# Performance work log

Hardware: AMD Instinct MI355X
Metric: run time of the kernel (lower is better)

## Reference

```python
import jax, jax.numpy as jnp
import numpy as np

N_NODES = 50000
N_EDGES = 800000
IN_CH = 64
HID = 128


def setup_inputs() -> dict:
    key = jax.random.key(0)
    ks = jax.random.split(key, 10)
    x = jax.random.normal(ks[0], (N_NODES, IN_CH), dtype=jnp.float32)
    edge_index = jax.random.randint(ks[1], (2, N_EDGES), 0, N_NODES, dtype=jnp.int64)
    def lin(k, fan_in, fan_out):
        bound = 1.0 / np.sqrt(fan_in)
        kw, kb = jax.random.split(k)
        W = jax.random.uniform(kw, (fan_in, fan_out), minval=-bound, maxval=bound, dtype=jnp.float32)
        b = jax.random.uniform(kb, (fan_out,), minval=-bound, maxval=bound, dtype=jnp.float32)
        return W, b
    W1a, b1a = lin(ks[2], 2 * IN_CH, HID)
    W1b, b1b = lin(ks[3], HID, HID)
    W2a, b2a = lin(ks[4], 2 * HID, HID)
    W2b, b2b = lin(ks[5], HID, HID)
    return {"x": x, "edge_index": edge_index,
            "W1a": W1a, "b1a": b1a, "W1b": W1b, "b1b": b1b,
            "W2a": W2a, "b2a": b2a, "W2b": W2b, "b2b": b2b}


def _edge_conv(x, src, dst, Wa, ba, Wb, bb):
    # PyG EdgeConv: message = MLP([x_i, x_j - x_i]), aggr = max at target i (dst)
    xi = x[dst]                                   # [E, C] target feats
    xj = x[src]                                   # [E, C] source feats
    m = jnp.concatenate([xi, xj - xi], axis=-1)   # [E, 2C]
    m = jax.nn.relu(m @ Wa + ba) @ Wb + bb        # [E, H]
    agg = jax.ops.segment_max(m, dst, num_segments=N_NODES)
    # nodes with no incoming edge -> 0 (torch_scatter fill value)
    return jnp.where(jnp.isfinite(agg), agg, 0.0)


def reference(x, edge_index, W1a, b1a, W1b, b1b, W2a, b2a, W2b, b2b):
    src = edge_index[0]
    dst = edge_index[1]
    h = _edge_conv(x, src, dst, W1a, b1a, W1b, b1b)
    h = jax.nn.relu(h)
    h = _edge_conv(h, src, dst, W2a, b2a, W2b, b2b)
    return h
```

## Files before the change

### kernel.cpp

```cpp
#include <hip/hip_runtime.h>
#include <stdint.h>

#define N_NODES 50000
#define N_EDGES 800000
#define HID 128
#define NWG_E (N_EDGES / 128)
#define XQ (NWG_E / 8)
#define XR (NWG_E % 8)
#define SCAN_B 196

#define ENC_NEG_INF 0x007FFFFFu

typedef short short8 __attribute__((ext_vector_type(8)));
typedef float f32x4 __attribute__((ext_vector_type(4)));

__device__ __forceinline__ unsigned enc_f32(float f) {
    unsigned u = __float_as_uint(f);
    return (u & 0x80000000u) ? ~u : (u | 0x80000000u);
}
__device__ __forceinline__ float dec_f32(unsigned e) {
    unsigned u = (e & 0x80000000u) ? (e & 0x7FFFFFFFu) : ~e;
    return __uint_as_float(u);
}
__device__ __forceinline__ unsigned short f2bf(float f) {
    unsigned u = __float_as_uint(f);
    unsigned r = (u + 0x7fffu + ((u >> 16) & 1u)) >> 16;
    return (unsigned short)r;
}
__device__ __forceinline__ float bf2f(unsigned short h) {
    return __uint_as_float(((unsigned)h) << 16);
}


__global__ void fill_u32(unsigned* __restrict__ p, int n, unsigned v) {
    int i = blockIdx.x * blockDim.x + threadIdx.x;
    int stride = gridDim.x * blockDim.x;
    for (; i < n; i += stride) p[i] = v;
}

__global__ void prep_wcat(const float* __restrict__ W, int K, float* __restrict__ WC) {
    int idx = blockIdx.x * 256 + threadIdx.x;
    if (idx >= K * 256) return;
    int k = idx >> 8, c = idx & 255;
    float v;
    if (c < 128) v = W[k * 128 + c] - W[(k + K) * 128 + c];
    else         v = W[(k + K) * 128 + (c - 128)];
    WC[idx] = v;
}

__global__ void prep_wfrag(const float* __restrict__ Wb, unsigned short* __restrict__ Wg) {
    int idx = blockIdx.x * 256 + threadIdx.x;
    int j = idx & 7, l = (idx >> 3) & 63, t = idx >> 9;
    int h = t >> 4, kt = (t >> 2) & 3, ntl = t & 3;
    int nt = 4 * h + ntl;
    int k = 32 * kt + 8 * (l >> 4) + j;
    int n = 16 * nt + (l & 15);
    Wg[idx] = f2bf(Wb[k * 128 + n]);
}

__global__ void prep_wfrag256(const float* __restrict__ WC, int K, unsigned short* __restrict__ Wg) {
    int idx = blockIdx.x * 256 + threadIdx.x;
    if (idx >= K * 256) return;
    int j = idx & 7, l = (idx >> 3) & 63, nt = (idx >> 9) & 15, kt = idx >> 13;
    int k = 32 * kt + 8 * (l >> 4) + j;
    int n = 16 * nt + (l & 15);
    float v = WC[k * 256 + n];
    unsigned short hi = f2bf(v);
    Wg[idx] = hi;
    Wg[K * 256 + idx] = f2bf(v - bf2f(hi));
}

__global__ void out_decode(unsigned* __restrict__ p, const float* __restrict__ bias, int n) {
    int i = blockIdx.x * blockDim.x + threadIdx.x;
    int stride = gridDim.x * blockDim.x;
    for (; i < n; i += stride) {
        unsigned e = p[i];
        float f = (e == ENC_NEG_INF) ? 0.0f : dec_f32(e) + bias[i & 127];
        ((float*)p)[i] = f;
    }
}


__global__ void hist_dst(const int* __restrict__ dst, unsigned* __restrict__ count) {
    int i = blockIdx.x * blockDim.x + threadIdx.x;
    if (i < N_EDGES) atomicAdd(&count[dst[i]], 1u);
}

__global__ __launch_bounds__(256) void scan_p1(const unsigned* __restrict__ count,
                                               unsigned* __restrict__ bsum) {
    __shared__ unsigned s[256];
    int t = threadIdx.x;
    int i = blockIdx.x * 256 + t;
    s[t] = (i < N_NODES) ? count[i] : 0u;
    __syncthreads();
    for (int off = 128; off > 0; off >>= 1) {
        if (t < off) s[t] += s[t + off];
        __syncthreads();
    }
    if (t == 0) bsum[blockIdx.x] = s[0];
}

__global__ __launch_bounds__(256) void scan_p2(unsigned* __restrict__ bsum) {
    __shared__ unsigned s[256];
    int t = threadIdx.x;
    unsigned v = (t < SCAN_B) ? bsum[t] : 0u;
    s[t] = v;
    __syncthreads();
    for (int off = 1; off < 256; off <<= 1) {
        unsigned x = (t >= off) ? s[t - off] : 0u;
        __syncthreads();
        s[t] += x;
        __syncthreads();
    }
    if (t < SCAN_B) bsum[t] = s[t] - v;
}

__global__ __launch_bounds__(256) void scan_p3(const unsigned* __restrict__ count,
                                               const unsigned* __restrict__ bsum,
                                               unsigned* __restrict__ cursor) {
    __shared__ unsigned s[256];
    int t = threadIdx.x;
    int i = blockIdx.x * 256 + t;
    unsigned v = (i < N_NODES) ? count[i] : 0u;
    s[t] = v;
    __syncthreads();
    for (int off = 1; off < 256; off <<= 1) {
        unsigned x = (t >= off) ? s[t - off] : 0u;
        __syncthreads();
        s[t] += x;
        __syncthreads();
    }
    if (i < N_NODES) cursor[i] = bsum[blockIdx.x] + s[t] - v;
}

__global__ void scatter_edges(const int* __restrict__ src, const int* __restrict__ dst,
                              unsigned* __restrict__ cursor,
                              int* __restrict__ ssrc, int* __restrict__ sdst) {
    int i = blockIdx.x * blockDim.x + threadIdx.x;
    if (i < N_EDGES) {
        int d = dst[i];
        unsigned p = atomicAdd(&cursor[d], 1u);
        ssrc[p] = src[i];
        sdst[p] = d;
    }
}

template<int DEC, int KT>
__global__ __launch_bounds__(256, 2) void gemm_uv_mfma(
        const void* __restrict__ A_,
        const unsigned short* __restrict__ Wg,
        const float* __restrict__ bprev,
        const float* __restrict__ bu,
        unsigned short* __restrict__ C,
        int M) {
    __shared__ char lds[KT * 8192];
    const int K = 32 * KT;
    int tid = threadIdx.x;
    int bx = blockIdx.x, by = blockIdx.y;
    int r0 = bx * 128;
    int w = tid >> 6, l = tid & 63;
    int q = l >> 4, m = l & 15;

    short8 ahi[2][KT];
#pragma unroll
    for (int mt = 0; mt < 2; ++mt) {
        int row = r0 + 32 * w + 16 * mt + m;
        bool ok = row < M;
#pragma unroll
        for (int kt = 0; kt < KT; ++kt) {
            float av[8] = {0.f, 0.f, 0.f, 0.f, 0.f, 0.f, 0.f, 0.f};
            if (ok) {
                if (DEC) {
                    const unsigned* Ar = (const unsigned*)A_ + (size_t)row * K + 32 * kt + 8 * q;
                    uint4 x0 = *(const uint4*)Ar;
                    uint4 x1 = *(const uint4*)(Ar + 4);
                    float4 g0 = *(const float4*)&bprev[32 * kt + 8 * q];
                    float4 g1 = *(const float4*)&bprev[32 * kt + 8 * q + 4];
                    av[0] = fmaxf(dec_f32(x0.x) + g0.x, 0.f);
                    av[1] = fmaxf(dec_f32(x0.y) + g0.y, 0.f);
                    av[2] = fmaxf(dec_f32(x0.z) + g0.z, 0.f);
                    av[3] = fmaxf(dec_f32(x0.w) + g0.w, 0.f);
                    av[4] = fmaxf(dec_f32(x1.x) + g1.x, 0.f);
                    av[5] = fmaxf(dec_f32(x1.y) + g1.y, 0.f);
                    av[6] = fmaxf(dec_f32(x1.z) + g1.z, 0.f);
                    av[7] = fmaxf(dec_f32(x1.w) + g1.w, 0.f);
                } else {
                    const float* Ar = (const float*)A_ + (size_t)row * K + 32 * kt + 8 * q;
                    float4 f0 = *(const float4*)Ar;
                    float4 f1 = *(const float4*)(Ar + 4);
                    av[0] = f0.x; av[1] = f0.y; av[2] = f0.z; av[3] = f0.w;
                    av[4] = f1.x; av[5] = f1.y; av[6] = f1.z; av[7] = f1.w;
                }
            }
            short8 hi;
#pragma unroll
            for (int j = 0; j < 8; ++j) hi[j] = (short)f2bf(av[j]);
            ahi[mt][kt] = hi;
        }
    }

    f32x4 acc[2][8];
#pragma unroll
    for (int mt = 0; mt < 2; ++mt)
#pragma unroll
        for (int nt = 0; nt < 8; ++nt)
            acc[mt][nt] = (f32x4){0.f, 0.f, 0.f, 0.f};

    const short8* bfr = (const short8*)lds;

#pragma unroll
    for (int pl = 0; pl < 2; ++pl) {
        if (pl) __syncthreads();
        {
            const float4* s4 = (const float4*)Wg + (size_t)pl * (K * 32);
            float4* d4 = (float4*)lds;
#pragma unroll
            for (int it = 0; it < 2 * KT; ++it) {
                int f = 256 * it + tid;
                int tl = f >> 6, fin = f & 63;
                int tg = (tl >> 3) * 16 + 8 * by + (tl & 7);
                d4[f] = s4[tg * 64 + fin];
            }
        }
        __syncthreads();
#pragma unroll
        for (int nt = 0; nt < 8; ++nt)
#pragma unroll
            for (int kt = 0; kt < KT; ++kt) {
                short8 b = bfr[(kt * 8 + nt) * 64 + l];
                acc[0][nt] = __builtin_amdgcn_mfma_f32_16x16x32_bf16(ahi[0][kt], b, acc[0][nt], 0, 0, 0);
                acc[1][nt] = __builtin_amdgcn_mfma_f32_16x16x32_bf16(ahi[1][kt], b, acc[1][nt], 0, 0, 0);
            }
    }

#pragma unroll
    for (int nt = 0; nt < 8; ++nt) {
        float bias = (by == 0) ? bu[16 * nt + m] : 0.f;
#pragma unroll
        for (int mt = 0; mt < 2; ++mt) {
            int rowb = r0 + 32 * w + 16 * mt + 4 * q;
#pragma unroll
            for (int r = 0; r < 4; ++r) {
                int row = rowb + r;
                if (row < M)
                    C[(size_t)row * 256 + 128 * by + 16 * nt + m] = f2bf(acc[mt][nt][r] + bias);
            }
        }
    }
}

__global__ __launch_bounds__(256, 5) void edge_mlp_mfma(
        const unsigned short* __restrict__ UV,
        const unsigned short* __restrict__ Wg,
        const int* __restrict__ ssrc,
        const int* __restrict__ sdst,
        unsigned* __restrict__ AGG) {
    __shared__ char lds[17408];
    __shared__ int sdst_s[128];
    int tid = threadIdx.x;
    int orig = blockIdx.x;
    int xcd = orig & 7, ii = orig >> 3;
    int wg = (xcd < XR) ? xcd * (XQ + 1) + ii : XR * (XQ + 1) + (xcd - XR) * XQ + ii;
    int e0 = wg * 128;
    int w = tid >> 6, l = tid & 63;
    int q = l >> 4, m = l & 15;

    if (tid < 128) sdst_s[tid] = sdst[e0 + tid];

    short8 ahi[2][4];
    {
        int eA = e0 + 32 * w + m;
        int d0 = sdst[eA], s0 = ssrc[eA];
        int d1 = sdst[eA + 16], s1 = ssrc[eA + 16];
#pragma unroll
        for (int mt = 0; mt < 2; ++mt) {
            int d = mt ? d1 : d0, s = mt ? s1 : s0;
            const short8* Ud = (const short8*)&UV[(size_t)d * 256];
            const short8* Vs = (const short8*)&UV[(size_t)s * 256 + 128];
            short8 u0 = Ud[q],      u1 = Ud[4 + q],  u2 = Ud[8 + q],  u3 = Ud[12 + q];
            short8 v0 = Vs[q],      v1 = Vs[4 + q],  v2 = Vs[8 + q],  v3 = Vs[12 + q];
            short8 ub[4] = {u0, u1, u2, u3};
            short8 vb[4] = {v0, v1, v2, v3};
#pragma unroll
            for (int kt = 0; kt < 4; ++kt) {
                short8 hi;
#pragma unroll
                for (int j = 0; j < 8; ++j) {
                    float t = bf2f((unsigned short)ub[kt][j]) + bf2f((unsigned short)vb[kt][j]);
                    hi[j] = (short)f2bf(fmaxf(t, 0.f));
                }
                ahi[mt][kt] = hi;
            }
        }
    }

    const short8* bfr = (const short8*)lds;
    float* M2 = (float*)lds;
    f32x4 acc[2][4];

#pragma unroll
    for (int h = 0; h < 2; ++h) {
        __syncthreads();
        {
            const float4* s4 = (const float4*)Wg + h * 1024;
            float4* d4 = (float4*)lds;
#pragma unroll
            for (int i = 0; i < 4; ++i) d4[tid + 256 * i] = s4[tid + 256 * i];
        }
        __syncthreads();
#pragma unroll
        for (int mt = 0; mt < 2; ++mt)
#pragma unroll
            for (int ntl = 0; ntl < 4; ++ntl)
                acc[mt][ntl] = (f32x4){0.f, 0.f, 0.f, 0.f};
#pragma unroll
        for (int ntl = 0; ntl < 4; ++ntl)
#pragma unroll
            for (int kt = 0; kt < 4; ++kt) {
                short8 b = bfr[(kt * 4 + ntl) * 64 + l];
                acc[0][ntl] = __builtin_amdgcn_mfma_f32_16x16x32_bf16(ahi[0][kt], b, acc[0][ntl], 0, 0, 0);
                acc[1][ntl] = __builtin_amdgcn_mfma_f32_16x16x32_bf16(ahi[1][kt], b, acc[1][ntl], 0, 0, 0);
            }

#pragma unroll
        for (int cn = 0; cn < 2; ++cn) {
            __syncthreads();
#pragma unroll
            for (int nt2 = 0; nt2 < 2; ++nt2) {
                int ntl = 2 * cn + nt2;
#pragma unroll
                for (int mt = 0; mt < 2; ++mt)
#pragma unroll
                    for (int r = 0; r < 4; ++r)
                        M2[(32 * w + 16 * mt + 4 * q + r) * 34 + 16 * nt2 + m] = acc[mt][ntl][r];
            }
            __syncthreads();
            {
                int c = tid & 31, g = tid >> 5;
                int eb = 16 * g;
                int cur = sdst_s[eb];
                float mx = -3.402823466e38f;
                for (int e2 = eb; e2 < eb + 16; ++e2) {
                    int de = sdst_s[e2];
                    if (de != cur) {
                        atomicMax(&AGG[(size_t)cur * 128 + 64 * h + 32 * cn + c], enc_f32(mx));
                        cur = de;
                        mx = -3.402823466e38f;
                    }
                    mx = fmaxf(mx, M2[e2 * 34 + c]);
                }
                atomicMax(&AGG[(size_t)cur * 128 + 64 * h + 32 * cn + c], enc_f32(mx));
            }
        }
    }
}


extern "C" void kernel_launch(void* const* d_in, const int* in_sizes, int n_in,
                              void* d_out, int out_size, void* d_ws, size_t ws_size,
                              hipStream_t stream) {
    const float* x   = (const float*)d_in[0];
    const int*   ei  = (const int*)d_in[1];
    const float* W1a = (const float*)d_in[2];
    const float* b1a = (const float*)d_in[3];
    const float* W1b = (const float*)d_in[4];
    const float* b1b = (const float*)d_in[5];
    const float* W2a = (const float*)d_in[6];
    const float* b2a = (const float*)d_in[7];
    const float* W2b = (const float*)d_in[8];
    const float* b2b = (const float*)d_in[9];
    const int* src = ei;
    const int* dst = ei + N_EDGES;

    char* ws = (char*)d_ws;
    unsigned short* UV    = (unsigned short*)ws;
    unsigned*       AGG1  = (unsigned*)(ws + 25600000);
    int*            ssrc  = (int*)(ws + 51200000);
    int*            sdst  = (int*)(ws + 54400000);
    unsigned*       count = (unsigned*)(ws + 57600000);
    unsigned*       cursor= (unsigned*)(ws + 57800000);
    unsigned short* Wg1   = (unsigned short*)(ws + 58000000);
    unsigned short* Wg2   = (unsigned short*)(ws + 58065536);
    float*          WC1   = (float*)(ws + 58131072);
    float*          WC2   = (float*)(ws + 58196608);
    unsigned short* WCg1  = (unsigned short*)(ws + 58327680);
    unsigned short* WCg2  = (unsigned short*)(ws + 58393216);
    unsigned*       bsum  = (unsigned*)(ws + 58655744);

    const int NH = N_NODES * HID;

    prep_wcat<<<64, 256, 0, stream>>>(W1a, 64, WC1);
    prep_wcat<<<128, 256, 0, stream>>>(W2a, 128, WC2);
    prep_wfrag<<<64, 256, 0, stream>>>(W1b, Wg1);
    prep_wfrag<<<64, 256, 0, stream>>>(W2b, Wg2);
    prep_wfrag256<<<64, 256, 0, stream>>>(WC1, 64, WCg1);
    prep_wfrag256<<<128, 256, 0, stream>>>(WC2, 128, WCg2);
    fill_u32<<<2048, 256, 0, stream>>>(AGG1, NH, ENC_NEG_INF);
    fill_u32<<<2048, 256, 0, stream>>>((unsigned*)d_out, NH, ENC_NEG_INF);
    fill_u32<<<196, 256, 0, stream>>>(count, N_NODES, 0u);

    hist_dst<<<3125, 256, 0, stream>>>(dst, count);
    scan_p1<<<SCAN_B, 256, 0, stream>>>(count, bsum);
    scan_p2<<<1, 256, 0, stream>>>(bsum);
    scan_p3<<<SCAN_B, 256, 0, stream>>>(count, bsum, cursor);
    scatter_edges<<<3125, 256, 0, stream>>>(src, dst, cursor, ssrc, sdst);

    gemm_uv_mfma<0, 2><<<dim3(391, 2), 256, 0, stream>>>(x, WCg1, nullptr, b1a, UV, N_NODES);
    edge_mlp_mfma<<<NWG_E, 256, 0, stream>>>(UV, Wg1, ssrc, sdst, AGG1);

    gemm_uv_mfma<1, 4><<<dim3(391, 2), 256, 0, stream>>>(AGG1, WCg2, b1b, b2a, UV, N_NODES);
    edge_mlp_mfma<<<NWG_E, 256, 0, stream>>>(UV, Wg2, ssrc, sdst, (unsigned*)d_out);
    out_decode<<<2048, 256, 0, stream>>>((unsigned*)d_out, b2b, NH);
}
```

Baseline: 317.8 us.

## Fuse setup kernels into one launch, batch edge gathers, lower occupancy bound

Nine small preparation launches (weight concatenation, fragment packing, buffer fills) are merged into one setup kernel that computes the concatenated weight values inline, so the intermediate WC buffers go away. The edge MLP kernel now issues all U/V row gathers for both edge tiles before any conversion, so more memory loads are in flight at once. Its launch bound drops from 5 to 4 waves per SIMD to make room for the extra registers. The aim is less launch overhead and better hiding of gather latency, at the cost of lower occupancy.

```diff
diff --git a/kernel.cpp b/kernel.cpp
--- a/kernel.cpp
+++ b/kernel.cpp
@@ -30,44 +30,56 @@
 __device__ __forceinline__ float bf2f(unsigned short h) {
     return __uint_as_float(((unsigned)h) << 16);
 }
-
-
-__global__ void fill_u32(unsigned* __restrict__ p, int n, unsigned v) {
-    int i = blockIdx.x * blockDim.x + threadIdx.x;
-    int stride = gridDim.x * blockDim.x;
-    for (; i < n; i += stride) p[i] = v;
-}
-
-__global__ void prep_wcat(const float* __restrict__ W, int K, float* __restrict__ WC) {
-    int idx = blockIdx.x * 256 + threadIdx.x;
-    if (idx >= K * 256) return;
-    int k = idx >> 8, c = idx & 255;
-    float v;
-    if (c < 128) v = W[k * 128 + c] - W[(k + K) * 128 + c];
-    else         v = W[(k + K) * 128 + (c - 128)];
-    WC[idx] = v;
-}
-
-__global__ void prep_wfrag(const float* __restrict__ Wb, unsigned short* __restrict__ Wg) {
-    int idx = blockIdx.x * 256 + threadIdx.x;
-    int j = idx & 7, l = (idx >> 3) & 63, t = idx >> 9;
-    int h = t >> 4, kt = (t >> 2) & 3, ntl = t & 3;
-    int nt = 4 * h + ntl;
-    int k = 32 * kt + 8 * (l >> 4) + j;
-    int n = 16 * nt + (l & 15);
-    Wg[idx] = f2bf(Wb[k * 128 + n]);
-}
-
-__global__ void prep_wfrag256(const float* __restrict__ WC, int K, unsigned short* __restrict__ Wg) {
-    int idx = blockIdx.x * 256 + threadIdx.x;
-    if (idx >= K * 256) return;
-    int j = idx & 7, l = (idx >> 3) & 63, nt = (idx >> 9) & 15, kt = idx >> 13;
-    int k = 32 * kt + 8 * (l >> 4) + j;
-    int n = 16 * nt + (l & 15);
-    float v = WC[k * 256 + n];
-    unsigned short hi = f2bf(v);
-    Wg[idx] = hi;
-    Wg[K * 256 + idx] = f2bf(v - bf2f(hi));
+__device__ __forceinline__ float wcat_val(const float* __restrict__ W, int K, int k, int n) {
+    return (n < 128) ? (W[k * 128 + n] - W[(k + K) * 128 + n]) : W[(k + K) * 128 + (n - 128)];
+}
+
+__global__ __launch_bounds__(256) void setup(
+        const float* __restrict__ W1a, const float* __restrict__ W1b,
+        const float* __restrict__ W2a, const float* __restrict__ W2b,
+        unsigned short* __restrict__ Wg1, unsigned short* __restrict__ Wg2,
+        unsigned short* __restrict__ WCg1, unsigned short* __restrict__ WCg2,
+        unsigned* __restrict__ AGG1, unsigned* __restrict__ OUT,
+        unsigned* __restrict__ count) {
+    int bid = blockIdx.x, tid = threadIdx.x;
+    const int NH = N_NODES * HID;
+
+    if (bid < 128) {
+        const float* Wb = (bid < 64) ? W1b : W2b;
+        unsigned short* Wg = (bid < 64) ? Wg1 : Wg2;
+        int idx = (bid & 63) * 256 + tid;
+        int j = idx & 7, l = (idx >> 3) & 63, t = idx >> 9;
+        int h = t >> 4, kt = (t >> 2) & 3, ntl = t & 3;
+        int nt = 4 * h + ntl;
+        int k = 32 * kt + 8 * (l >> 4) + j;
+        int n = 16 * nt + (l & 15);
+        Wg[idx] = f2bf(Wb[k * 128 + n]);
+    } else if (bid < 192) {
+        int idx = (bid - 128) * 256 + tid;
+        int j = idx & 7, l = (idx >> 3) & 63, nt = (idx >> 9) & 15, kt = idx >> 13;
+        int k = 32 * kt + 8 * (l >> 4) + j;
+        int n = 16 * nt + (l & 15);
+        float v = wcat_val(W1a, 64, k, n);
+        unsigned short hi = f2bf(v);
+        WCg1[idx] = hi;
+        WCg1[64 * 256 + idx] = f2bf(v - bf2f(hi));
+    } else if (bid < 320) {
+        int idx = (bid - 192) * 256 + tid;
+        int j = idx & 7, l = (idx >> 3) & 63, nt = (idx >> 9) & 15, kt = idx >> 13;
+        int k = 32 * kt + 8 * (l >> 4) + j;
+        int n = 16 * nt + (l & 15);
+        float v = wcat_val(W2a, 128, k, n);
+        unsigned short hi = f2bf(v);
+        WCg2[idx] = hi;
+        WCg2[128 * 256 + idx] = f2bf(v - bf2f(hi));
+    }
+
+    int total = 2 * NH + N_NODES;
+    for (int i = bid * 256 + tid; i < total; i += gridDim.x * 256) {
+        if (i < NH) AGG1[i] = ENC_NEG_INF;
+        else if (i < 2 * NH) OUT[i - NH] = ENC_NEG_INF;
+        else count[i - 2 * NH] = 0u;
+    }
 }
 
 __global__ void out_decode(unsigned* __restrict__ p, const float* __restrict__ bias, int n) {
@@ -249,7 +261,7 @@
     }
 }
 
-__global__ __launch_bounds__(256, 5) void edge_mlp_mfma(
+__global__ __launch_bounds__(256, 4) void edge_mlp_mfma(
         const unsigned short* __restrict__ UV,
         const unsigned short* __restrict__ Wg,
         const int* __restrict__ ssrc,
@@ -272,26 +284,30 @@
         int eA = e0 + 32 * w + m;
         int d0 = sdst[eA], s0 = ssrc[eA];
         int d1 = sdst[eA + 16], s1 = ssrc[eA + 16];
-#pragma unroll
-        for (int mt = 0; mt < 2; ++mt) {
-            int d = mt ? d1 : d0, s = mt ? s1 : s0;
-            const short8* Ud = (const short8*)&UV[(size_t)d * 256];
-            const short8* Vs = (const short8*)&UV[(size_t)s * 256 + 128];
-            short8 u0 = Ud[q],      u1 = Ud[4 + q],  u2 = Ud[8 + q],  u3 = Ud[12 + q];
-            short8 v0 = Vs[q],      v1 = Vs[4 + q],  v2 = Vs[8 + q],  v3 = Vs[12 + q];
-            short8 ub[4] = {u0, u1, u2, u3};
-            short8 vb[4] = {v0, v1, v2, v3};
+        const short8* Ud0 = (const short8*)&UV[(size_t)d0 * 256];
+        const short8* Vs0 = (const short8*)&UV[(size_t)s0 * 256 + 128];
+        const short8* Ud1 = (const short8*)&UV[(size_t)d1 * 256];
+        const short8* Vs1 = (const short8*)&UV[(size_t)s1 * 256 + 128];
+        short8 ub[2][4], vb[2][4];
+#pragma unroll
+        for (int kt = 0; kt < 4; ++kt) {
+            ub[0][kt] = Ud0[4 * kt + q];
+            vb[0][kt] = Vs0[4 * kt + q];
+            ub[1][kt] = Ud1[4 * kt + q];
+            vb[1][kt] = Vs1[4 * kt + q];
+        }
+#pragma unroll
+        for (int mt = 0; mt < 2; ++mt)
 #pragma unroll
             for (int kt = 0; kt < 4; ++kt) {
                 short8 hi;
 #pragma unroll
                 for (int j = 0; j < 8; ++j) {
-                    float t = bf2f((unsigned short)ub[kt][j]) + bf2f((unsigned short)vb[kt][j]);
+                    float t = bf2f((unsigned short)ub[mt][kt][j]) + bf2f((unsigned short)vb[mt][kt][j]);
                     hi[j] = (short)f2bf(fmaxf(t, 0.f));
                 }
                 ahi[mt][kt] = hi;
             }
-        }
     }
 
     const short8* bfr = (const short8*)lds;
@@ -381,23 +397,14 @@
     unsigned*       cursor= (unsigned*)(ws + 57800000);
     unsigned short* Wg1   = (unsigned short*)(ws + 58000000);
     unsigned short* Wg2   = (unsigned short*)(ws + 58065536);
-    float*          WC1   = (float*)(ws + 58131072);
-    float*          WC2   = (float*)(ws + 58196608);
     unsigned short* WCg1  = (unsigned short*)(ws + 58327680);
     unsigned short* WCg2  = (unsigned short*)(ws + 58393216);
     unsigned*       bsum  = (unsigned*)(ws + 58655744);
 
     const int NH = N_NODES * HID;
 
-    prep_wcat<<<64, 256, 0, stream>>>(W1a, 64, WC1);
-    prep_wcat<<<128, 256, 0, stream>>>(W2a, 128, WC2);
-    prep_wfrag<<<64, 256, 0, stream>>>(W1b, Wg1);
-    prep_wfrag<<<64, 256, 0, stream>>>(W2b, Wg2);
-    prep_wfrag256<<<64, 256, 0, stream>>>(WC1, 64, WCg1);
-    prep_wfrag256<<<128, 256, 0, stream>>>(WC2, 128, WCg2);
-    fill_u32<<<2048, 256, 0, stream>>>(AGG1, NH, ENC_NEG_INF);
-    fill_u32<<<2048, 256, 0, stream>>>((unsigned*)d_out, NH, ENC_NEG_INF);
-    fill_u32<<<196, 256, 0, stream>>>(count, N_NODES, 0u);
+    setup<<<2048, 256, 0, stream>>>(W1a, W1b, W2a, W2b, Wg1, Wg2, WCg1, WCg2,
+                                    AGG1, (unsigned*)d_out, count);
 
     hist_dst<<<3125, 256, 0, stream>>>(dst, count);
     scan_p1<<<SCAN_B, 256, 0, stream>>>(count, bsum);
```

New measurement: 314.9 us. About the same (-0.9%).
